# Performance work log

Measured on AMD Instinct MI355X. Metric: run time of the kernel, lower is better.

Reference implementation:

```python
import jax, jax.numpy as jnp
import numpy as np

N, C, RATIO, POS_P = 8192, 5000, 3.0, 0.01


def setup_inputs() -> dict:
    key = jax.random.key(0)
    k1, k2 = jax.random.split(key)
    pred = jax.random.normal(k1, (N, C), dtype=jnp.float32)
    # sparse binary multilabel targets (~50 positives per row)
    target = (jax.random.uniform(k2, (N, C)) < POS_P).astype(jnp.float32)
    return {"pred": pred, "target": target}


def reference(pred, target):
    # pred, target: [N, C]
    num_classes = pred.shape[-1]
    pos = jnp.sum(target, axis=-1)                         # [N] positives per row
    neg = jnp.minimum(pos * RATIO, num_classes - pos)      # [N] hard negatives to keep

    # hard-negative selection: top-neg entries of softmax(pred) - target
    prob = jax.nn.softmax(pred, axis=-1)
    score = prob - target                                  # positives pushed below negatives
    # rank 0 = largest score (matches torch.topk ordering)
    ranks = jnp.argsort(jnp.argsort(-score, axis=-1), axis=-1)
    hard = (ranks < neg[:, None]).astype(pred.dtype)       # [N, C]
    mask = jnp.maximum(target, hard)                       # mask = target.clone(); mask[topk]=1

    # old-torch multilabel_soft_margin_loss(size_average=False) == weighted BCE sum:
    # -(y*log sigmoid(x) + (1-y)*log(1-sigmoid(x))) = softplus(x) - y*x
    bce = jax.nn.softplus(pred) - target * pred
    loss = jnp.sum(mask * bce)
    return loss / jnp.sum(target)
```

## Files before the change

### kernel.cpp

```cpp
#include <hip/hip_runtime.h>
#include <stdint.h>


#define C_DIM 5000
#define C4_DIM 1250
#define BLK 256
#define SCAP 1024
#define CUT 1.25f
#define NSLOT 64

__device__ __forceinline__ float sp_f(float x) {
    return fmaxf(x, 0.0f) + __logf(1.0f + __expf(-fabsf(x)));
}
__device__ __forceinline__ uint32_t mono_u(float x) {
    uint32_t b = __float_as_uint(x);
    return b ^ ((b & 0x80000000u) ? 0xFFFFFFFFu : 0x80000000u);
}
__device__ __forceinline__ float unmono_f(uint32_t u) {
    uint32_t b = (u & 0x80000000u) ? (u ^ 0x80000000u) : ~u;
    return __uint_as_float(b);
}
__device__ __forceinline__ int vbin_of(float x) {
    int v = (int)((x - CUT) * 128.0f);
    return v > 255 ? 255 : (v < 0 ? 0 : v);
}

__device__ __forceinline__ void find_bin(const unsigned int* hist, int kp, int tid, int* s_sel) {
    if (tid < 64) {
        int c0 = (int)hist[4 * tid + 0];
        int c1 = (int)hist[4 * tid + 1];
        int c2 = (int)hist[4 * tid + 2];
        int c3 = (int)hist[4 * tid + 3];
        int lsum = c0 + c1 + c2 + c3;
        int s = lsum;
        #pragma unroll
        for (int off = 1; off < 64; off <<= 1) {
            int o = __shfl_down(s, off);
            if (tid + off < 64) s += o;
        }
        int above = s - lsum;
        if (above < kp && kp <= s) {
            int b, ab;
            if (kp <= above + c3)                { b = 4 * tid + 3; ab = above; }
            else if (kp <= above + c3 + c2)      { b = 4 * tid + 2; ab = above + c3; }
            else if (kp <= above + c3 + c2 + c1) { b = 4 * tid + 1; ab = above + c3 + c2; }
            else                                 { b = 4 * tid;     ab = above + c3 + c2 + c1; }
            s_sel[0] = b;
            s_sel[1] = ab;
        }
    }
}

__global__ __launch_bounds__(BLK, 8) void hardneg_kernel(
    const float* __restrict__ pred, const float* __restrict__ target,
    char* __restrict__ ws)
{
    __shared__ uint32_t s_buf[SCAP];
    __shared__ unsigned int hist[256];
    __shared__ int i_scr[4];
    __shared__ float f_scr[4];
    __shared__ int s_sel[2];
    __shared__ int s_misc[4];
    __shared__ int s_cnt;
    __shared__ uint32_t s_tiny[64];

    const int tid = threadIdx.x;
    const int lane = tid & 63;
    const int wv = tid >> 6;
    const int row = blockIdx.x;
    const float4* pr4 = (const float4*)(pred + (size_t)row * C_DIM);
    const float4* tg4 = (const float4*)(target + (size_t)row * C_DIM);

    hist[tid] = 0;
    if (tid < 4) { i_scr[tid] = 0; s_misc[tid] = 0; }
    if (tid == 0) s_cnt = 0;
    __syncthreads();

    float acc = 0.0f;
    int pos_cnt = 0;

    for (int c = 0; c < 5; ++c) {
        int i = tid + c * BLK;
        float4 p = {0.f, 0.f, 0.f, 0.f}, t = {0.f, 0.f, 0.f, 0.f};
        if (i < C4_DIM) { p = pr4[i]; t = tg4[i]; }
        float xs[4] = {p.x, p.y, p.z, p.w};
        float ts[4] = {t.x, t.y, t.z, t.w};
        float cv0 = 0.f, cv1 = 0.f, cv2 = 0.f, cv3 = 0.f;
        int nc = 0;
        #pragma unroll
        for (int j = 0; j < 4; ++j) {
            float x = xs[j];
            if (ts[j] != 0.0f) {
                pos_cnt++;
                acc += sp_f(x) - x;
            } else if (x > CUT) {
                atomicAdd(&hist[vbin_of(x)], 1u);
                if (nc == 0) cv0 = x; else if (nc == 1) cv1 = x;
                else if (nc == 2) cv2 = x; else cv3 = x;
                ++nc;
            }
        }
        unsigned pfx = (unsigned)nc;
        #pragma unroll
        for (int off = 1; off < 64; off <<= 1) {
            unsigned o = (unsigned)__shfl_up((int)pfx, off);
            if (lane >= off) pfx += o;
        }
        int base = 0;
        if (lane == 63) base = atomicAdd(&s_cnt, (int)pfx);
        base = __shfl(base, 63);
        int w = base + (int)pfx - nc;
        if (nc > 0 && w + 0 < SCAP) s_buf[w + 0] = __float_as_uint(cv0) ^ 0x80000000u;
        if (nc > 1 && w + 1 < SCAP) s_buf[w + 1] = __float_as_uint(cv1) ^ 0x80000000u;
        if (nc > 2 && w + 2 < SCAP) s_buf[w + 2] = __float_as_uint(cv2) ^ 0x80000000u;
        if (nc > 3 && w + 3 < SCAP) s_buf[w + 3] = __float_as_uint(cv3) ^ 0x80000000u;
    }

    int v = pos_cnt;
    #pragma unroll
    for (int off = 32; off; off >>= 1) v += __shfl_down(v, off);
    if (lane == 0) i_scr[wv] = v;
    __syncthreads();
    const int pos_total = i_scr[0] + i_scr[1] + i_scr[2] + i_scr[3];
    const int k = min(3 * pos_total, C_DIM - pos_total);
    const int cnt = s_cnt;
    if (k == 0) return;

    uint32_t tu;
    int n_at;
    const bool fb = (k > cnt) || (cnt > SCAP);

    if (!fb) {
        find_bin(hist, k, tid, s_sel);
        __syncthreads();
        const int bv = s_sel[0];
        int kp = k - s_sel[1];

        for (int i = tid; i < cnt; i += BLK) {
            uint32_t u = s_buf[i];
            if (vbin_of(unmono_f(u)) == bv) {
                int idx = atomicAdd(&s_misc[0], 1);
                if (idx < 64) s_tiny[idx] = u;
            }
        }
        __syncthreads();
        const int tcnt = s_misc[0];

        if (tcnt <= 64) {
            if (tid < 64) {
                uint32_t ul = (lane < tcnt) ? s_tiny[lane] : 0u;
                int sg = 0, eq = 0;
                for (int j = 0; j < tcnt; ++j) {
                    uint32_t uj = (uint32_t)__shfl((int)ul, j);
                    sg += (uj > ul);
                    eq += (uj == ul);
                }
                if (lane < tcnt && sg < kp && kp <= sg + eq) {
                    s_misc[1] = (int)ul;
                    s_misc[2] = kp - sg;
                }
            }
            __syncthreads();
            tu = (uint32_t)s_misc[1];
            n_at = s_misc[2];
        } else {
            uint32_t prefix = 0;
            for (int r = 0; r < 4; ++r) {
                const int shift = 24 - 8 * r;
                __syncthreads();
                hist[tid] = 0;
                __syncthreads();
                for (int i = tid; i < cnt; i += BLK) {
                    uint32_t u = s_buf[i];
                    bool match = (vbin_of(unmono_f(u)) == bv);
                    if (r > 0) match = match && ((u >> (shift + 8)) == (prefix >> (shift + 8)));
                    if (match) atomicAdd(&hist[(u >> shift) & 255u], 1u);
                }
                __syncthreads();
                find_bin(hist, kp, tid, s_sel);
                __syncthreads();
                prefix |= ((uint32_t)s_sel[0]) << shift;
                kp -= s_sel[1];
            }
            tu = prefix;
            n_at = kp;
        }

        for (int i = tid; i < cnt; i += BLK) {
            uint32_t u = s_buf[i];
            if (u > tu) acc += sp_f(unmono_f(u));
        }
    } else {
        uint32_t prefix = 0;
        int kq = k;
        for (int r = 0; r < 4; ++r) {
            const int shift = 24 - 8 * r;
            __syncthreads();
            hist[tid] = 0;
            __syncthreads();
            for (int i = tid; i < C4_DIM; i += BLK) {
                float4 p = pr4[i];
                float4 t = tg4[i];
                float xs[4] = {p.x, p.y, p.z, p.w};
                float ts[4] = {t.x, t.y, t.z, t.w};
                #pragma unroll
                for (int j = 0; j < 4; ++j) {
                    if (ts[j] == 0.0f) {
                        uint32_t u = mono_u(xs[j]);
                        bool m = (r == 0) || ((u >> (shift + 8)) == (prefix >> (shift + 8)));
                        if (m) atomicAdd(&hist[(u >> shift) & 255u], 1u);
                    }
                }
            }
            __syncthreads();
            find_bin(hist, kq, tid, s_sel);
            __syncthreads();
            prefix |= ((uint32_t)s_sel[0]) << shift;
            kq -= s_sel[1];
        }
        tu = prefix;
        n_at = kq;
        for (int i = tid; i < C4_DIM; i += BLK) {
            float4 p = pr4[i];
            float4 t = tg4[i];
            float xs[4] = {p.x, p.y, p.z, p.w};
            float ts[4] = {t.x, t.y, t.z, t.w};
            #pragma unroll
            for (int j = 0; j < 4; ++j) {
                if (ts[j] == 0.0f) {
                    uint32_t u = mono_u(xs[j]);
                    if (u > tu) acc += sp_f(xs[j]);
                }
            }
        }
    }

    #pragma unroll
    for (int off = 32; off; off >>= 1) acc += __shfl_down(acc, off);
    if (lane == 0) f_scr[wv] = acc;
    __syncthreads();
    if (tid == 0) {
        float rowsum = f_scr[0] + f_scr[1] + f_scr[2] + f_scr[3]
                     + (float)n_at * sp_f(unmono_f(tu));
        char* slot = ws + (size_t)(row & (NSLOT - 1)) * 16;
        atomicAdd((double*)slot, (double)rowsum);
        atomicAdd((float*)(slot + 8), (float)pos_total);
    }
}

__global__ void hardneg_finalize(const char* __restrict__ ws, float* __restrict__ out)
{
    const int l = threadIdx.x;
    double n = *(const double*)(ws + (size_t)l * 16);
    float d = *(const float*)(ws + (size_t)l * 16 + 8);
    #pragma unroll
    for (int off = 32; off; off >>= 1) {
        n += __shfl_down(n, off);
        d += __shfl_down(d, off);
    }
    if (l == 0) out[0] = (d > 0.0f) ? (float)(n / (double)d) : 0.0f;
}

extern "C" void kernel_launch(void* const* d_in, const int* in_sizes, int n_in,
                              void* d_out, int out_size, void* d_ws, size_t ws_size,
                              hipStream_t stream) {
    const float* pred = (const float*)d_in[0];
    const float* target = (const float*)d_in[1];
    float* out = (float*)d_out;
    char* ws = (char*)d_ws;

    hipMemsetAsync(ws, 0, NSLOT * 16, stream);

    const int nrows = in_sizes[0] / C_DIM;
    hardneg_kernel<<<nrows, BLK, 0, stream>>>(pred, target, ws);
    hardneg_finalize<<<1, 64, 0, stream>>>(ws, out);
}
```

Measured before the change: 337.6 us.

## Defer softplus and histogram work out of the streaming load loop

The first pass now only loads, classifies and compacts values. Positives go into a new shared buffer and candidates go through per-element shared atomics instead of a wave prefix scan. Positive softplus terms and the candidate histogram are computed afterwards from shared memory, with a global reload fallback if positives overflow the buffer. The load loop is fully unrolled so the loads can be issued together, and launch bounds drop to 4 blocks per SM to allow more registers. The cost is heavier contention on the single shared counters and possibly lower occupancy.

```diff
diff --git a/kernel.cpp b/kernel.cpp
--- a/kernel.cpp
+++ b/kernel.cpp
@@ -6,6 +6,7 @@
 #define C4_DIM 1250
 #define BLK 256
 #define SCAP 1024
+#define PCAP 512
 #define CUT 1.25f
 #define NSLOT 64
 
@@ -51,17 +52,18 @@
     }
 }
 
-__global__ __launch_bounds__(BLK, 8) void hardneg_kernel(
+__global__ __launch_bounds__(BLK, 4) void hardneg_kernel(
     const float* __restrict__ pred, const float* __restrict__ target,
     char* __restrict__ ws)
 {
     __shared__ uint32_t s_buf[SCAP];
+    __shared__ uint32_t s_pbuf[PCAP];
     __shared__ unsigned int hist[256];
-    __shared__ int i_scr[4];
     __shared__ float f_scr[4];
     __shared__ int s_sel[2];
     __shared__ int s_misc[4];
     __shared__ int s_cnt;
+    __shared__ int s_pcnt;
     __shared__ uint32_t s_tiny[64];
 
     const int tid = threadIdx.x;
@@ -72,65 +74,64 @@
     const float4* tg4 = (const float4*)(target + (size_t)row * C_DIM);
 
     hist[tid] = 0;
-    if (tid < 4) { i_scr[tid] = 0; s_misc[tid] = 0; }
-    if (tid == 0) s_cnt = 0;
+    if (tid < 4) s_misc[tid] = 0;
+    if (tid == 0) { s_cnt = 0; s_pcnt = 0; }
     __syncthreads();
 
-    float acc = 0.0f;
-    int pos_cnt = 0;
-
+    #pragma unroll
     for (int c = 0; c < 5; ++c) {
         int i = tid + c * BLK;
-        float4 p = {0.f, 0.f, 0.f, 0.f}, t = {0.f, 0.f, 0.f, 0.f};
-        if (i < C4_DIM) { p = pr4[i]; t = tg4[i]; }
-        float xs[4] = {p.x, p.y, p.z, p.w};
-        float ts[4] = {t.x, t.y, t.z, t.w};
-        float cv0 = 0.f, cv1 = 0.f, cv2 = 0.f, cv3 = 0.f;
-        int nc = 0;
-        #pragma unroll
-        for (int j = 0; j < 4; ++j) {
-            float x = xs[j];
-            if (ts[j] != 0.0f) {
-                pos_cnt++;
-                acc += sp_f(x) - x;
-            } else if (x > CUT) {
-                atomicAdd(&hist[vbin_of(x)], 1u);
-                if (nc == 0) cv0 = x; else if (nc == 1) cv1 = x;
-                else if (nc == 2) cv2 = x; else cv3 = x;
-                ++nc;
-            }
-        }
-        unsigned pfx = (unsigned)nc;
-        #pragma unroll
-        for (int off = 1; off < 64; off <<= 1) {
-            unsigned o = (unsigned)__shfl_up((int)pfx, off);
-            if (lane >= off) pfx += o;
-        }
-        int base = 0;
-        if (lane == 63) base = atomicAdd(&s_cnt, (int)pfx);
-        base = __shfl(base, 63);
-        int w = base + (int)pfx - nc;
-        if (nc > 0 && w + 0 < SCAP) s_buf[w + 0] = __float_as_uint(cv0) ^ 0x80000000u;
-        if (nc > 1 && w + 1 < SCAP) s_buf[w + 1] = __float_as_uint(cv1) ^ 0x80000000u;
-        if (nc > 2 && w + 2 < SCAP) s_buf[w + 2] = __float_as_uint(cv2) ^ 0x80000000u;
-        if (nc > 3 && w + 3 < SCAP) s_buf[w + 3] = __float_as_uint(cv3) ^ 0x80000000u;
-    }
-
-    int v = pos_cnt;
-    #pragma unroll
-    for (int off = 32; off; off >>= 1) v += __shfl_down(v, off);
-    if (lane == 0) i_scr[wv] = v;
+        if (c < 4 || i < C4_DIM) {
+            float4 p = pr4[i];
+            float4 t = tg4[i];
+            float xs[4] = {p.x, p.y, p.z, p.w};
+            float ts[4] = {t.x, t.y, t.z, t.w};
+            #pragma unroll
+            for (int j = 0; j < 4; ++j) {
+                float x = xs[j];
+                if (ts[j] != 0.0f) {
+                    int ip = atomicAdd(&s_pcnt, 1);
+                    if (ip < PCAP) s_pbuf[ip] = __float_as_uint(x);
+                } else if (x > CUT) {
+                    int ic = atomicAdd(&s_cnt, 1);
+                    if (ic < SCAP) s_buf[ic] = __float_as_uint(x) ^ 0x80000000u;
+                }
+            }
+        }
+    }
     __syncthreads();
-    const int pos_total = i_scr[0] + i_scr[1] + i_scr[2] + i_scr[3];
+
+    const int pos_total = s_pcnt;
+    const int cnt = s_cnt;
     const int k = min(3 * pos_total, C_DIM - pos_total);
-    const int cnt = s_cnt;
     if (k == 0) return;
+
+    float acc = 0.0f;
+    if (pos_total <= PCAP) {
+        for (int i = tid; i < pos_total; i += BLK) {
+            float x = __uint_as_float(s_pbuf[i]);
+            acc += sp_f(x) - x;
+        }
+    } else {
+        for (int i = tid; i < C4_DIM; i += BLK) {
+            float4 p = pr4[i];
+            float4 t = tg4[i];
+            float xs[4] = {p.x, p.y, p.z, p.w};
+            float ts[4] = {t.x, t.y, t.z, t.w};
+            #pragma unroll
+            for (int j = 0; j < 4; ++j)
+                if (ts[j] != 0.0f) acc += sp_f(xs[j]) - xs[j];
+        }
+    }
 
     uint32_t tu;
     int n_at;
     const bool fb = (k > cnt) || (cnt > SCAP);
 
     if (!fb) {
+        for (int i = tid; i < cnt; i += BLK)
+            atomicAdd(&hist[vbin_of(unmono_f(s_buf[i]))], 1u);
+        __syncthreads();
         find_bin(hist, k, tid, s_sel);
         __syncthreads();
         const int bv = s_sel[0];
@@ -227,10 +228,7 @@
             float ts[4] = {t.x, t.y, t.z, t.w};
             #pragma unroll
             for (int j = 0; j < 4; ++j) {
-                if (ts[j] == 0.0f) {
-                    uint32_t u = mono_u(xs[j]);
-                    if (u > tu) acc += sp_f(xs[j]);
-                }
+                if (ts[j] == 0.0f && mono_u(xs[j]) > tu) acc += sp_f(xs[j]);
             }
         }
     }
```

Result: no change. 337.2 us (-0.1%).
